# Optimization experiments

Hardware: AMD Instinct MI355X
Metric: run time of the kernel (lower is better)

The kernel has to match this reference:

```python
import jax, jax.numpy as jnp
import numpy as np

N_HEADS = 16
D_QKV = 128
THETA = 10000.0


def setup_inputs() -> dict:
    key = jax.random.key(0)
    k1, k2, k3 = jax.random.split(key, 3)
    B, L, d_model = 2, 2048, 2048
    X = jax.random.normal(k1, (B, L, d_model), jnp.float32)
    # torch Linear weight is (out,in); we store the transposed (in,out) layout so y = X @ W
    W_qkv = jax.random.normal(k2, (d_model, 3 * N_HEADS * D_QKV), jnp.float32) / np.sqrt(d_model)
    W_out = jax.random.normal(k3, (N_HEADS * D_QKV, d_model), jnp.float32) / np.sqrt(N_HEADS * D_QKV)
    return {"X": X, "W_qkv": W_qkv, "W_out": W_out}


def _rope(x, cos, sin):
    # interleaved-pair RoPE (rotary-embedding-torch style): pairs are (x[2i], x[2i+1])
    x1 = x[..., 0::2]
    x2 = x[..., 1::2]
    out = jnp.stack([x1 * cos - x2 * sin, x1 * sin + x2 * cos], axis=-1)
    return out.reshape(x.shape)


def reference(X, W_qkv, W_out):
    B, L, _ = X.shape
    H, D = N_HEADS, D_QKV
    # fused QKV projection; layout per head is [q|k|v] of size 3*D (matches 'b l (h ddd)')
    qkv = (X @ W_qkv).reshape(B, L, H, 3 * D).transpose(0, 2, 1, 3)  # b h l 3d
    Q, K, V = jnp.split(qkv, 3, axis=-1)                              # each b h l d
    inv_freq = 1.0 / (THETA ** (jnp.arange(0, D, 2, dtype=jnp.float32) / D))
    ang = jnp.arange(L, dtype=jnp.float32)[:, None] * inv_freq[None, :]  # (L, D/2)
    cos, sin = jnp.cos(ang), jnp.sin(ang)
    Q = _rope(Q, cos, sin)
    K = _rope(K, cos, sin)
    # causal SDPA
    scores = jnp.einsum('bhqd,bhkd->bhqk', Q, K) / jnp.sqrt(jnp.float32(D))
    causal = jnp.tril(jnp.ones((L, L), dtype=bool))
    scores = jnp.where(causal, scores, -jnp.inf)
    attn = jax.nn.softmax(scores, axis=-1)
    out = jnp.einsum('bhqk,bhkd->bqhd', attn, V).reshape(B, L, H * D)
    return out @ W_out
```

## Files before the change

kernel.cpp:

```cpp
#include <hip/hip_runtime.h>

typedef __bf16 bf16x8 __attribute__((ext_vector_type(8)));
typedef float f32x4 __attribute__((ext_vector_type(4)));

#define LSEQ 2048

__device__ __forceinline__ unsigned short f2b(float f){
  unsigned u = __builtin_bit_cast(unsigned, f);
  u += 0x7FFFu + ((u >> 16) & 1u);
  return (unsigned short)(u >> 16);
}
__device__ __forceinline__ float b2f(unsigned short h){
  unsigned u = ((unsigned)h) << 16;
  return __builtin_bit_cast(float, u);
}
__device__ __forceinline__ unsigned cvt_pk_bf16(float lo, float hi){
  unsigned r;
  asm("v_cvt_pk_bf16_f32 %0, %1, %2" : "=v"(r) : "v"(lo), "v"(hi));
  return r;
}

typedef __attribute__((address_space(1))) const unsigned int glb_u32;
typedef __attribute__((address_space(3))) unsigned int lds_u32;
__device__ __forceinline__ void gld_lds16(const void* g, void* l){
  __builtin_amdgcn_global_load_lds((glb_u32*)g, (lds_u32*)l, 16, 0, 0);
}

__global__ __launch_bounds__(256) void cvt_f32_bf16(const float* __restrict__ in,
                                                    unsigned short* __restrict__ out){
  int tid = blockIdx.x * 256 + threadIdx.x;
  float4 v = reinterpret_cast<const float4*>(in)[tid];
  ushort4 o;
  o.x = f2b(v.x); o.y = f2b(v.y); o.z = f2b(v.z); o.w = f2b(v.w);
  reinterpret_cast<ushort4*>(out)[tid] = o;
}

__global__ __launch_bounds__(256) void transpose_cvt(const float* __restrict__ in,
                                                     unsigned short* __restrict__ out,
                                                     int R, int C){
  __shared__ float t[32][33];
  int c0 = blockIdx.x * 32, r0 = blockIdx.y * 32;
  int tx = threadIdx.x, ty = threadIdx.y;
  #pragma unroll
  for (int i = 0; i < 4; i++){
    int r = ty + i*8;
    t[r][tx] = in[(size_t)(r0 + r) * C + c0 + tx];
  }
  __syncthreads();
  #pragma unroll
  for (int i = 0; i < 4; i++){
    int c = ty + i*8;
    out[(size_t)(c0 + c) * R + r0 + tx] = f2b(t[tx][c]);
  }
}

__global__ __launch_bounds__(256) void trig_init(float* __restrict__ cosT,
                                                 float* __restrict__ sinT){
  int tid = blockIdx.x * 256 + threadIdx.x;
  int i = tid & 63; int l = tid >> 6;
  float invf = powf(10000.0f, -((float)(2*i)) / 128.0f);
  float ang = (float)l * invf;
  cosT[tid] = cosf(ang);
  sinT[tid] = sinf(ang);
}

__global__ __launch_bounds__(256) void rope_qk(const unsigned short* __restrict__ qkv,
                                               const float* __restrict__ cosT,
                                               const float* __restrict__ sinT,
                                               unsigned short* __restrict__ Qr,
                                               unsigned short* __restrict__ Kr){
  int tid = blockIdx.x * 256 + threadIdx.x;
  int i  = tid & 63;
  int l  = (tid >> 6) & (LSEQ - 1);
  int bh = tid >> 17;
  int b = bh >> 4, h = bh & 15;
  size_t base = (size_t)(b*LSEQ + l) * 6144 + h*384;
  float c = cosT[l*64 + i], s = sinT[l*64 + i];
  float q1 = b2f(qkv[base + 2*i]),       q2 = b2f(qkv[base + 2*i + 1]);
  float k1 = b2f(qkv[base + 128 + 2*i]), k2 = b2f(qkv[base + 128 + 2*i + 1]);
  const float qs = 0.12751691f;
  size_t ob = ((size_t)bh*LSEQ + l) * 128;
  Qr[ob + 2*i]     = f2b((q1*c - q2*s) * qs);
  Qr[ob + 2*i + 1] = f2b((q1*s + q2*c) * qs);
  Kr[ob + 2*i]     = f2b(k1*c - k2*s);
  Kr[ob + 2*i + 1] = f2b(k1*s + k2*c);
}

__global__ __launch_bounds__(256) void vtrans(const unsigned short* __restrict__ qkv,
                                              unsigned short* __restrict__ Vt){
  __shared__ unsigned short t[64][65];
  int d0 = blockIdx.x * 64, l0 = blockIdx.y * 64, bh = blockIdx.z;
  int b = bh >> 4, h = bh & 15;
  int tx = threadIdx.x, ty = threadIdx.y;
  #pragma unroll
  for (int i = 0; i < 16; i++){
    int lr = ty + i*4;
    t[lr][tx] = qkv[(size_t)(b*LSEQ + l0 + lr) * 6144 + h*384 + 256 + d0 + tx];
  }
  __syncthreads();
  #pragma unroll
  for (int i = 0; i < 16; i++){
    int dr = ty + i*4;
    Vt[(size_t)(bh*128 + d0 + dr) * LSEQ + l0 + tx] = t[tx][dr];
  }
}

template<bool BF16_OUT>
__global__ __launch_bounds__(256) void gemm_bt(const unsigned short* __restrict__ A,
                                               const unsigned short* __restrict__ Bt,
                                               void* __restrict__ Cp,
                                               int M, int N, int K){
  __shared__ __align__(16) unsigned short As[128*64];
  __shared__ __align__(16) unsigned short Bs[128*64];
  int m0 = blockIdx.y * 128, n0 = blockIdx.x * 128;
  int tid = threadIdx.x, lane = tid & 63, wave = tid >> 6;
  int wm = wave >> 1, wn = wave & 1;
  int lr = lane & 15, lh = lane >> 4;
  int r8 = lane >> 3;
  int cg = (lane & 7) ^ r8;
  f32x4 acc[4][4];
  #pragma unroll
  for (int a = 0; a < 4; a++)
    #pragma unroll
    for (int bb = 0; bb < 4; bb++)
      acc[a][bb] = (f32x4){0.f, 0.f, 0.f, 0.f};

  const unsigned short* Abase = A  + (size_t)(m0 + wave*32 + r8)*K + cg*8;
  const unsigned short* Bbase = Bt + (size_t)(n0 + wave*32 + r8)*K + cg*8;

  int nk = K >> 6;
  for (int k0 = 0; k0 < nk; k0++){
    __syncthreads();
    #pragma unroll
    for (int i = 0; i < 4; i++){
      gld_lds16(Abase + (size_t)i*8*K + k0*64, &As[(wave*32 + i*8)*64]);
      gld_lds16(Bbase + (size_t)i*8*K + k0*64, &Bs[(wave*32 + i*8)*64]);
    }
    __syncthreads();
    #pragma unroll
    for (int kk = 0; kk < 2; kk++){
      bf16x8 af[4], bfg[4];
      #pragma unroll
      for (int f = 0; f < 4; f++){
        int ra = wm*64 + f*16 + lr;
        af[f]  = *reinterpret_cast<const bf16x8*>(&As[ra*64 + (((kk*4 + lh) ^ (ra & 7)) * 8)]);
        int rb = wn*64 + f*16 + lr;
        bfg[f] = *reinterpret_cast<const bf16x8*>(&Bs[rb*64 + (((kk*4 + lh) ^ (rb & 7)) * 8)]);
      }
      __builtin_amdgcn_s_setprio(1);
      #pragma unroll
      for (int fm = 0; fm < 4; fm++)
        #pragma unroll
        for (int fn = 0; fn < 4; fn++)
          acc[fm][fn] = __builtin_amdgcn_mfma_f32_16x16x32_bf16(af[fm], bfg[fn], acc[fm][fn], 0, 0, 0);
      __builtin_amdgcn_s_setprio(0);
    }
  }
  #pragma unroll
  for (int fm = 0; fm < 4; fm++)
    #pragma unroll
    for (int fn = 0; fn < 4; fn++)
      #pragma unroll
      for (int r = 0; r < 4; r++){
        int row = m0 + wm*64 + fm*16 + lh*4 + r;
        int col = n0 + wn*64 + fn*16 + lr;
        float v = acc[fm][fn][r];
        if (BF16_OUT) ((unsigned short*)Cp)[(size_t)row*N + col] = f2b(v);
        else          ((float*)Cp)[(size_t)row*N + col] = v;
      }
}

__global__ __launch_bounds__(256) void attn_kernel(const unsigned short* __restrict__ Qr,
                                                   const unsigned short* __restrict__ Kr,
                                                   const unsigned short* __restrict__ Vt,
                                                   unsigned short* __restrict__ aout){
  __shared__ __align__(16) unsigned short Ks[2][64*128];
  __shared__ __align__(16) unsigned short Vs[2][128*64];
  __shared__ __align__(16) unsigned short Ps[4][2][16*64];
  int bh = blockIdx.x;
  int y = blockIdx.y;
  int qi = (y < 8) ? (15 - y) : (y - 8);
  int q0 = qi * 128;
  int tid = threadIdx.x;
  int wave = tid >> 6, lane = tid & 63;
  int lr = lane & 15, lh = lane >> 4;
  int b = bh >> 4, h = bh & 15;

  bf16x8 qf[2][4];
  #pragma unroll
  for (int g = 0; g < 2; g++){
    const unsigned short* Qb = Qr + ((size_t)bh*LSEQ + q0 + wave*32 + g*16 + lr) * 128;
    #pragma unroll
    for (int kc = 0; kc < 4; kc++)
      qf[g][kc] = *reinterpret_cast<const bf16x8*>(Qb + kc*32 + lh*8);
  }

  float m_i[2], l_i[2];
  f32x4 o[2][8];
  #pragma unroll
  for (int g = 0; g < 2; g++){ m_i[g] = -__builtin_inff(); l_i[g] = 0.f; }
  #pragma unroll
  for (int g = 0; g < 2; g++)
    #pragma unroll
    for (int nd = 0; nd < 8; nd++) o[g][nd] = (f32x4){0.f, 0.f, 0.f, 0.f};

  const unsigned short* Kbh = Kr + (size_t)bh*LSEQ*128;
  const unsigned short* Vbh = Vt + (size_t)bh*128*LSEQ;
  int klrow = lane >> 4;
  int vlrow = lane >> 3;
  int vg = (lane & 7) ^ vlrow;
  int srcb = (lane & 48) + ((lane >> 2) & 12);

  int ntiles = (q0 >> 6) + 2;

  #pragma unroll
  for (int i = 0; i < 4; i++){
    int rk = wave*16 + i*4 + klrow;
    int gk = (lane & 15) ^ (rk & 7);
    gld_lds16(Kbh + (size_t)rk*128 + gk*8, &Ks[0][(wave*16 + i*4)*128]);
    int rv = wave*32 + i*8 + vlrow;
    gld_lds16(Vbh + (size_t)rv*LSEQ + vg*8, &Vs[0][(wave*32 + i*8)*64]);
  }
  __syncthreads();

  int cur = 0;
  for (int t = 0; t < ntiles; t++){
    if (t + 1 < ntiles){
      int kv1 = (t + 1) * 64;
      #pragma unroll
      for (int i = 0; i < 4; i++){
        int rk = wave*16 + i*4 + klrow;
        int gk = (lane & 15) ^ (rk & 7);
        gld_lds16(Kbh + (size_t)(kv1 + rk)*128 + gk*8, &Ks[cur^1][(wave*16 + i*4)*128]);
        int rv = wave*32 + i*8 + vlrow;
        gld_lds16(Vbh + (size_t)rv*LSEQ + kv1 + vg*8, &Vs[cur^1][(wave*32 + i*8)*64]);
      }
    }
    int kv0 = t * 64;

    f32x4 s[2][4];
    #pragma unroll
    for (int g = 0; g < 2; g++)
      #pragma unroll
      for (int nc = 0; nc < 4; nc++)
        s[g][nc] = (f32x4){0.f, 0.f, 0.f, 0.f};
    __builtin_amdgcn_s_setprio(1);
    #pragma unroll
    for (int nc = 0; nc < 4; nc++){
      int n = nc*16 + lr;
      #pragma unroll
      for (int kc = 0; kc < 4; kc++){
        bf16x8 kf = *reinterpret_cast<const bf16x8*>(&Ks[cur][n*128 + (((kc*4 + lh) ^ (n & 7)) * 8)]);
        s[0][nc] = __builtin_amdgcn_mfma_f32_16x16x32_bf16(kf, qf[0][kc], s[0][nc], 0, 0, 0);
        s[1][nc] = __builtin_amdgcn_mfma_f32_16x16x32_bf16(kf, qf[1][kc], s[1][nc], 0, 0, 0);
      }
    }
    __builtin_amdgcn_s_setprio(0);

    if (t >= ntiles - 2){
      #pragma unroll
      for (int g = 0; g < 2; g++)
        #pragma unroll
        for (int nc = 0; nc < 4; nc++)
          #pragma unroll
          for (int r = 0; r < 4; r++){
            int kv = kv0 + nc*16 + lh*4 + r;
            int q  = q0 + wave*32 + g*16 + lr;
            if (kv > q) s[g][nc][r] = -__builtin_inff();
          }
    }

    #pragma unroll
    for (int g = 0; g < 2; g++){
      float pm = -__builtin_inff();
      #pragma unroll
      for (int nc = 0; nc < 4; nc++)
        pm = fmaxf(pm, fmaxf(fmaxf(s[g][nc][0], s[g][nc][1]), fmaxf(s[g][nc][2], s[g][nc][3])));
      pm = fmaxf(pm, __shfl_xor(pm, 16, 64));
      pm = fmaxf(pm, __shfl_xor(pm, 32, 64));
      float mn = fmaxf(m_i[g], pm);
      float al = exp2f(m_i[g] - mn);
      m_i[g] = mn;
      float rs = 0.f;
      unsigned w[8];
      #pragma unroll
      for (int nc = 0; nc < 4; nc++){
        float p0 = exp2f(s[g][nc][0] - mn), p1 = exp2f(s[g][nc][1] - mn);
        float p2 = exp2f(s[g][nc][2] - mn), p3 = exp2f(s[g][nc][3] - mn);
        rs += (p0 + p1) + (p2 + p3);
        w[nc*2]     = cvt_pk_bf16(p0, p1);
        w[nc*2 + 1] = cvt_pk_bf16(p2, p3);
      }
      rs += __shfl_xor(rs, 16, 64);
      rs += __shfl_xor(rs, 32, 64);
      l_i[g] = l_i[g]*al + rs;
      float al_r[4];
      #pragma unroll
      for (int r = 0; r < 4; r++) al_r[r] = __shfl(al, srcb + r, 64);
      #pragma unroll
      for (int nd = 0; nd < 8; nd++)
        #pragma unroll
        for (int r = 0; r < 4; r++)
          o[g][nd][r] *= al_r[r];
      #pragma unroll
      for (int nc = 0; nc < 4; nc++)
        #pragma unroll
        for (int hh = 0; hh < 2; hh++){
          int kvg = nc*2 + (lh >> 1);
          int klo = (lh & 1)*4 + 2*hh;
          *reinterpret_cast<unsigned*>(&Ps[wave][g][lr*64 + ((kvg ^ (lr & 7)) << 3) + klo]) = w[nc*2 + hh];
        }
    }

    __builtin_amdgcn_s_setprio(1);
    #pragma unroll
    for (int kc = 0; kc < 2; kc++){
      bf16x8 pa0 = *reinterpret_cast<const bf16x8*>(&Ps[wave][0][lr*64 + (((kc*4 + lh) ^ (lr & 7)) << 3)]);
      bf16x8 pa1 = *reinterpret_cast<const bf16x8*>(&Ps[wave][1][lr*64 + (((kc*4 + lh) ^ (lr & 7)) << 3)]);
      #pragma unroll
      for (int nd = 0; nd < 8; nd++){
        int d = nd*16 + lr;
        bf16x8 vf = *reinterpret_cast<const bf16x8*>(&Vs[cur][d*64 + (((kc*4 + lh) ^ (d & 7)) << 3)]);
        o[0][nd] = __builtin_amdgcn_mfma_f32_16x16x32_bf16(pa0, vf, o[0][nd], 0, 0, 0);
        o[1][nd] = __builtin_amdgcn_mfma_f32_16x16x32_bf16(pa1, vf, o[1][nd], 0, 0, 0);
      }
    }
    __builtin_amdgcn_s_setprio(0);

    __syncthreads();
    cur ^= 1;
  }

  #pragma unroll
  for (int g = 0; g < 2; g++){
    float inv = 1.0f / l_i[g];
    float inv_r[4];
    #pragma unroll
    for (int r = 0; r < 4; r++) inv_r[r] = __shfl(inv, srcb + r, 64);
    #pragma unroll
    for (int nd = 0; nd < 8; nd++)
      #pragma unroll
      for (int r = 0; r < 4; r++){
        int q = q0 + wave*32 + g*16 + lh*4 + r;
        aout[((size_t)b*LSEQ + q)*2048 + h*128 + nd*16 + lr] = f2b(o[g][nd][r] * inv_r[r]);
      }
  }
}

extern "C" void kernel_launch(void* const* d_in, const int* in_sizes, int n_in,
                              void* d_out, int out_size, void* d_ws, size_t ws_size,
                              hipStream_t stream){
  const float* X  = (const float*)d_in[0];
  const float* Wq = (const float*)d_in[1];
  const float* Wo = (const float*)d_in[2];
  float* out = (float*)d_out;
  char* ws = (char*)d_ws;
  unsigned short* Xb   = (unsigned short*)(ws + 0);
  unsigned short* Wt   = (unsigned short*)(ws + 16777216);
  unsigned short* Wot  = (unsigned short*)(ws + 41943040);
  unsigned short* QKV  = (unsigned short*)(ws + 50331648);
  unsigned short* Kr   = (unsigned short*)(ws + 100663296);
  unsigned short* Vt   = (unsigned short*)(ws + 117440512);
  float* cosT          = (float*)(ws + 134217728);
  float* sinT          = (float*)(ws + 134742016);
  unsigned short* Qr   = Xb;
  unsigned short* Aout = QKV;

  cvt_f32_bf16<<<8192, 256, 0, stream>>>(X, Xb);
  transpose_cvt<<<dim3(192, 64), dim3(32, 8), 0, stream>>>(Wq, Wt, 2048, 6144);
  transpose_cvt<<<dim3(64, 64),  dim3(32, 8), 0, stream>>>(Wo, Wot, 2048, 2048);
  trig_init<<<512, 256, 0, stream>>>(cosT, sinT);
  gemm_bt<true><<<dim3(48, 32), 256, 0, stream>>>(Xb, Wt, (void*)QKV, 4096, 6144, 2048);
  rope_qk<<<16384, 256, 0, stream>>>(QKV, cosT, sinT, Qr, Kr);
  vtrans<<<dim3(2, 32, 32), dim3(64, 4), 0, stream>>>(QKV, Vt);
  attn_kernel<<<dim3(32, 16), 256, 0, stream>>>(Qr, Kr, Vt, Aout);
  gemm_bt<false><<<dim3(16, 32), 256, 0, stream>>>(Aout, Wot, (void*)out, 4096, 2048, 2048);
}
```

Before: 420.6 us.

## Rewrite attention inner loop with 32x32 MFMA and in-register P transpose

Switches the flash-attention kernel from 16x16x32 to 32x32x16 bf16 MFMA tiles, so each wave handles 32 query rows as a single group. The P matrix is rearranged into the A-operand layout with v_permlane32_swap in registers instead of being staged through LDS. The kernel also adds a lazy rescale that only updates the running max and rescales O when some row max grows by more than 8 (log2 units), and sets launch_bounds occupancy to 2 blocks. The goal is fewer LDS round-trips, fewer shuffles and fewer MFMA issues per tile. The cost is higher register pressure and reliance on the thresholded rescale staying numerically safe.

```diff
diff --git a/kernel.cpp b/kernel.cpp
--- a/kernel.cpp
+++ b/kernel.cpp
@@ -2,6 +2,8 @@
 
 typedef __bf16 bf16x8 __attribute__((ext_vector_type(8)));
 typedef float f32x4 __attribute__((ext_vector_type(4)));
+typedef float f32x16 __attribute__((ext_vector_type(16)));
+typedef unsigned u32x4 __attribute__((ext_vector_type(4)));
 
 #define LSEQ 2048
 
@@ -170,46 +172,38 @@
       }
 }
 
-__global__ __launch_bounds__(256) void attn_kernel(const unsigned short* __restrict__ Qr,
-                                                   const unsigned short* __restrict__ Kr,
-                                                   const unsigned short* __restrict__ Vt,
-                                                   unsigned short* __restrict__ aout){
+__global__ __launch_bounds__(256, 2) void attn_kernel(const unsigned short* __restrict__ Qr,
+                                                      const unsigned short* __restrict__ Kr,
+                                                      const unsigned short* __restrict__ Vt,
+                                                      unsigned short* __restrict__ aout){
   __shared__ __align__(16) unsigned short Ks[2][64*128];
   __shared__ __align__(16) unsigned short Vs[2][128*64];
-  __shared__ __align__(16) unsigned short Ps[4][2][16*64];
   int bh = blockIdx.x;
   int y = blockIdx.y;
   int qi = (y < 8) ? (15 - y) : (y - 8);
   int q0 = qi * 128;
   int tid = threadIdx.x;
   int wave = tid >> 6, lane = tid & 63;
-  int lr = lane & 15, lh = lane >> 4;
+  int ql = lane & 31;
+  int hi = lane >> 5;
   int b = bh >> 4, h = bh & 15;
 
-  bf16x8 qf[2][4];
-  #pragma unroll
-  for (int g = 0; g < 2; g++){
-    const unsigned short* Qb = Qr + ((size_t)bh*LSEQ + q0 + wave*32 + g*16 + lr) * 128;
-    #pragma unroll
-    for (int kc = 0; kc < 4; kc++)
-      qf[g][kc] = *reinterpret_cast<const bf16x8*>(Qb + kc*32 + lh*8);
-  }
-
-  float m_i[2], l_i[2];
-  f32x4 o[2][8];
-  #pragma unroll
-  for (int g = 0; g < 2; g++){ m_i[g] = -__builtin_inff(); l_i[g] = 0.f; }
-  #pragma unroll
-  for (int g = 0; g < 2; g++)
-    #pragma unroll
-    for (int nd = 0; nd < 8; nd++) o[g][nd] = (f32x4){0.f, 0.f, 0.f, 0.f};
+  bf16x8 qf[8];
+  const unsigned short* Qb = Qr + ((size_t)bh*LSEQ + q0 + wave*32 + ql) * 128 + hi*8;
+  #pragma unroll
+  for (int ks = 0; ks < 8; ks++)
+    qf[ks] = *reinterpret_cast<const bf16x8*>(Qb + ks*16);
+
+  float m_i = -1.0e38f, l_i = 0.f;
+  f32x16 o[4];
+  #pragma unroll
+  for (int nd = 0; nd < 4; nd++) o[nd] = (f32x16)(0.f);
 
   const unsigned short* Kbh = Kr + (size_t)bh*LSEQ*128;
   const unsigned short* Vbh = Vt + (size_t)bh*128*LSEQ;
   int klrow = lane >> 4;
   int vlrow = lane >> 3;
   int vg = (lane & 7) ^ vlrow;
-  int srcb = (lane & 48) + ((lane >> 2) & 12);
 
   int ntiles = (q0 >> 6) + 2;
 
@@ -238,91 +232,90 @@
     }
     int kv0 = t * 64;
 
-    f32x4 s[2][4];
-    #pragma unroll
-    for (int g = 0; g < 2; g++)
-      #pragma unroll
-      for (int nc = 0; nc < 4; nc++)
-        s[g][nc] = (f32x4){0.f, 0.f, 0.f, 0.f};
+    f32x16 sa0 = (f32x16)(0.f), sa1 = (f32x16)(0.f);
     __builtin_amdgcn_s_setprio(1);
     #pragma unroll
-    for (int nc = 0; nc < 4; nc++){
-      int n = nc*16 + lr;
-      #pragma unroll
-      for (int kc = 0; kc < 4; kc++){
-        bf16x8 kf = *reinterpret_cast<const bf16x8*>(&Ks[cur][n*128 + (((kc*4 + lh) ^ (n & 7)) * 8)]);
-        s[0][nc] = __builtin_amdgcn_mfma_f32_16x16x32_bf16(kf, qf[0][kc], s[0][nc], 0, 0, 0);
-        s[1][nc] = __builtin_amdgcn_mfma_f32_16x16x32_bf16(kf, qf[1][kc], s[1][nc], 0, 0, 0);
-      }
+    for (int ks = 0; ks < 8; ks++){
+      int g = 2*ks + hi;
+      bf16x8 kf0 = *reinterpret_cast<const bf16x8*>(&Ks[cur][ql*128 + ((g ^ (ql & 7)) * 8)]);
+      bf16x8 kf1 = *reinterpret_cast<const bf16x8*>(&Ks[cur][(32 + ql)*128 + ((g ^ ((32 + ql) & 7)) * 8)]);
+      sa0 = __builtin_amdgcn_mfma_f32_32x32x16_bf16(kf0, qf[ks], sa0, 0, 0, 0);
+      sa1 = __builtin_amdgcn_mfma_f32_32x32x16_bf16(kf1, qf[ks], sa1, 0, 0, 0);
     }
     __builtin_amdgcn_s_setprio(0);
 
     if (t >= ntiles - 2){
-      #pragma unroll
-      for (int g = 0; g < 2; g++)
-        #pragma unroll
-        for (int nc = 0; nc < 4; nc++)
-          #pragma unroll
-          for (int r = 0; r < 4; r++){
-            int kv = kv0 + nc*16 + lh*4 + r;
-            int q  = q0 + wave*32 + g*16 + lr;
-            if (kv > q) s[g][nc][r] = -__builtin_inff();
-          }
-    }
-
-    #pragma unroll
-    for (int g = 0; g < 2; g++){
-      float pm = -__builtin_inff();
-      #pragma unroll
-      for (int nc = 0; nc < 4; nc++)
-        pm = fmaxf(pm, fmaxf(fmaxf(s[g][nc][0], s[g][nc][1]), fmaxf(s[g][nc][2], s[g][nc][3])));
-      pm = fmaxf(pm, __shfl_xor(pm, 16, 64));
-      pm = fmaxf(pm, __shfl_xor(pm, 32, 64));
-      float mn = fmaxf(m_i[g], pm);
-      float al = exp2f(m_i[g] - mn);
-      m_i[g] = mn;
-      float rs = 0.f;
-      unsigned w[8];
-      #pragma unroll
-      for (int nc = 0; nc < 4; nc++){
-        float p0 = exp2f(s[g][nc][0] - mn), p1 = exp2f(s[g][nc][1] - mn);
-        float p2 = exp2f(s[g][nc][2] - mn), p3 = exp2f(s[g][nc][3] - mn);
-        rs += (p0 + p1) + (p2 + p3);
-        w[nc*2]     = cvt_pk_bf16(p0, p1);
-        w[nc*2 + 1] = cvt_pk_bf16(p2, p3);
-      }
-      rs += __shfl_xor(rs, 16, 64);
-      rs += __shfl_xor(rs, 32, 64);
-      l_i[g] = l_i[g]*al + rs;
-      float al_r[4];
-      #pragma unroll
-      for (int r = 0; r < 4; r++) al_r[r] = __shfl(al, srcb + r, 64);
-      #pragma unroll
-      for (int nd = 0; nd < 8; nd++)
-        #pragma unroll
-        for (int r = 0; r < 4; r++)
-          o[g][nd][r] *= al_r[r];
-      #pragma unroll
-      for (int nc = 0; nc < 4; nc++)
-        #pragma unroll
-        for (int hh = 0; hh < 2; hh++){
-          int kvg = nc*2 + (lh >> 1);
-          int klo = (lh & 1)*4 + 2*hh;
-          *reinterpret_cast<unsigned*>(&Ps[wave][g][lr*64 + ((kvg ^ (lr & 7)) << 3) + klo]) = w[nc*2 + hh];
-        }
-    }
+      int q = q0 + wave*32 + ql;
+      #pragma unroll
+      for (int r = 0; r < 16; r++){
+        int kvb = kv0 + (r & 3) + 8*(r >> 2) + 4*hi;
+        if (kvb > q)      sa0[r] = -1.0e38f;
+        if (kvb + 32 > q) sa1[r] = -1.0e38f;
+      }
+    }
+
+    float pm = -1.0e38f;
+    #pragma unroll
+    for (int r = 0; r < 16; r++) pm = fmaxf(pm, fmaxf(sa0[r], sa1[r]));
+    pm = fmaxf(pm, __shfl_xor(pm, 32, 64));
+
+    if (__any(pm > m_i + 8.0f)){
+      float mn = fmaxf(m_i, pm);
+      float al = exp2f(m_i - mn);
+      m_i = mn;
+      l_i *= al;
+      #pragma unroll
+      for (int r = 0; r < 16; r++){
+        int qsrc = (r & 3) + 8*(r >> 2) + 4*hi;
+        float alr = __shfl(al, qsrc, 64);
+        o[0][r] *= alr; o[1][r] *= alr; o[2][r] *= alr; o[3][r] *= alr;
+      }
+    }
+
+    float ps = 0.f;
+    unsigned wlo[2][4], whi[2][4];
+    #pragma unroll
+    for (int a = 0; a < 4; a++){
+      float p0 = exp2f(sa0[4*a]     - m_i);
+      float p1 = exp2f(sa0[4*a + 1] - m_i);
+      float p2 = exp2f(sa0[4*a + 2] - m_i);
+      float p3 = exp2f(sa0[4*a + 3] - m_i);
+      ps += (p0 + p1) + (p2 + p3);
+      wlo[0][a] = cvt_pk_bf16(p0, p1);
+      whi[0][a] = cvt_pk_bf16(p2, p3);
+      float p4 = exp2f(sa1[4*a]     - m_i);
+      float p5 = exp2f(sa1[4*a + 1] - m_i);
+      float p6 = exp2f(sa1[4*a + 2] - m_i);
+      float p7 = exp2f(sa1[4*a + 3] - m_i);
+      ps += (p4 + p5) + (p6 + p7);
+      wlo[1][a] = cvt_pk_bf16(p4, p5);
+      whi[1][a] = cvt_pk_bf16(p6, p7);
+    }
+    ps += __shfl_xor(ps, 32, 64);
+    l_i += ps;
+
+    bf16x8 pa[4];
+    #pragma unroll
+    for (int h2 = 0; h2 < 2; h2++)
+      #pragma unroll
+      for (int a0 = 0; a0 < 4; a0 += 2){
+        unsigned x  = wlo[h2][a0], y  = wlo[h2][a0 + 1];
+        asm("v_permlane32_swap_b32 %0, %1" : "+v"(x), "+v"(y));
+        unsigned x2 = whi[h2][a0], y2 = whi[h2][a0 + 1];
+        asm("v_permlane32_swap_b32 %0, %1" : "+v"(x2), "+v"(y2));
+        u32x4 w4 = (u32x4){x, x2, y, y2};
+        pa[2*h2 + (a0 >> 1)] = __builtin_bit_cast(bf16x8, w4);
+      }
 
     __builtin_amdgcn_s_setprio(1);
     #pragma unroll
-    for (int kc = 0; kc < 2; kc++){
-      bf16x8 pa0 = *reinterpret_cast<const bf16x8*>(&Ps[wave][0][lr*64 + (((kc*4 + lh) ^ (lr & 7)) << 3)]);
-      bf16x8 pa1 = *reinterpret_cast<const bf16x8*>(&Ps[wave][1][lr*64 + (((kc*4 + lh) ^ (lr & 7)) << 3)]);
-      #pragma unroll
-      for (int nd = 0; nd < 8; nd++){
-        int d = nd*16 + lr;
-        bf16x8 vf = *reinterpret_cast<const bf16x8*>(&Vs[cur][d*64 + (((kc*4 + lh) ^ (d & 7)) << 3)]);
-        o[0][nd] = __builtin_amdgcn_mfma_f32_16x16x32_bf16(pa0, vf, o[0][nd], 0, 0, 0);
-        o[1][nd] = __builtin_amdgcn_mfma_f32_16x16x32_bf16(pa1, vf, o[1][nd], 0, 0, 0);
+    for (int ks = 0; ks < 4; ks++){
+      int g = 2*ks + hi;
+      #pragma unroll
+      for (int nd = 0; nd < 4; nd++){
+        int dr = nd*32 + ql;
+        bf16x8 vf = *reinterpret_cast<const bf16x8*>(&Vs[cur][dr*64 + ((g ^ (dr & 7)) * 8)]);
+        o[nd] = __builtin_amdgcn_mfma_f32_32x32x16_bf16(pa[ks], vf, o[nd], 0, 0, 0);
       }
     }
     __builtin_amdgcn_s_setprio(0);
@@ -331,19 +324,17 @@
     cur ^= 1;
   }
 
-  #pragma unroll
-  for (int g = 0; g < 2; g++){
-    float inv = 1.0f / l_i[g];
-    float inv_r[4];
-    #pragma unroll
-    for (int r = 0; r < 4; r++) inv_r[r] = __shfl(inv, srcb + r, 64);
-    #pragma unroll
-    for (int nd = 0; nd < 8; nd++)
-      #pragma unroll
-      for (int r = 0; r < 4; r++){
-        int q = q0 + wave*32 + g*16 + lh*4 + r;
-        aout[((size_t)b*LSEQ + q)*2048 + h*128 + nd*16 + lr] = f2b(o[g][nd][r] * inv_r[r]);
-      }
+  float inv = 1.0f / l_i;
+  #pragma unroll
+  for (int r = 0; r < 16; r++){
+    int qsrc = (r & 3) + 8*(r >> 2) + 4*hi;
+    float invr = __shfl(inv, qsrc, 64);
+    int q = q0 + wave*32 + qsrc;
+    size_t rowb = ((size_t)b*LSEQ + q)*2048 + h*128 + ql;
+    aout[rowb]      = f2b(o[0][r] * invr);
+    aout[rowb + 32] = f2b(o[1][r] * invr);
+    aout[rowb + 64] = f2b(o[2][r] * invr);
+    aout[rowb + 96] = f2b(o[3][r] * invr);
   }
 }
 
```

Measured after the change: 380.8 us. 9.5% less time.
